# Performance work log

Hardware: AMD Instinct MI355X
Metric: run time of the kernel (lower is better)

Reference implementation:

```python
import jax, jax.numpy as jnp
import numpy as np

B, D, K = 8192, 2048, 2048  # batch, input dim, output_dim (must be equal: k==d required by call())


def setup_inputs() -> dict:
    key = jax.random.key(0)
    k1, k2, k3, k4 = jax.random.split(key, 4)
    lim_w = float(np.sqrt(6.0 / (K + D)))        # glorot_uniform for W (k,d)
    lim_v = float(np.sqrt(6.0 / (2 * D + K)))    # glorot_uniform for V (2d,k)
    return {
        "e1": jax.random.normal(k1, (B, D), jnp.float32),
        "e2": jax.random.normal(k2, (B, D), jnp.float32),
        "W": jax.random.uniform(k3, (K, D), jnp.float32, -lim_w, lim_w),
        "V": jax.random.uniform(k4, (2 * D, K), jnp.float32, -lim_v, lim_v),
        "b": jnp.zeros((K,), jnp.float32),
    }


def reference(e1, e2, W, V, b):
    # Faithful translation of the active call() of NeuralTensorDiagLayer.
    # call() tiles flatten(e1) k times and reshapes to (B, d, k); index algebra
    # shows x[p, q, r] = e1[(p*d+q)%B, r] * e2[(p*d+q)%B, r] * W[q, r]
    # (requires k == d for the W broadcast), then mean over the last axis (size k).
    # Equivalent efficient form: u = ((e1*e2) @ W.T)/k, then gather rows (p*d+q)%B.
    bsz, d = e1.shape
    k = W.shape[0]
    ff = jnp.concatenate([e1, e2], axis=-1) @ V              # (B, k) feedforward GEMM
    u = ((e1 * e2) @ W.T) / k                                # (B, k) diag bilinear, mean over k
    cols = jnp.arange(k)[None, :]                            # (1, k)
    rows = (jnp.arange(bsz)[:, None] * d + cols) % bsz       # (B, k) batch-mixing index from tile/reshape
    z = u[rows, cols]                                        # (B, k)
    return jnp.tanh(z + ff + b)
```

## Files before the change

kernel.cpp:

```cpp
#include <hip/hip_runtime.h>
#include <hip/hip_bf16.h>

typedef __bf16 bf16;
typedef bf16 bf16x8 __attribute__((ext_vector_type(8)));
typedef bf16 bf16x4 __attribute__((ext_vector_type(4)));
typedef float f32x4 __attribute__((ext_vector_type(4)));

#define AS1 __attribute__((address_space(1)))
#define AS3 __attribute__((address_space(3)))

__device__ __forceinline__ void gload_lds16(const void* g, void* l) {
    __builtin_amdgcn_global_load_lds((const AS1 void*)g, (AS3 void*)l, 16, 0, 0);
}

__device__ __forceinline__ float tanh_fast(float x) {
    float xx = fminf(fmaxf(x, -15.0f), 15.0f);
    float e = __expf(2.0f * xx);
    return (e - 1.0f) / (e + 1.0f);
}

__global__ __launch_bounds__(256) void conv_x_zs(
    const float* __restrict__ e1, const float* __restrict__ e2,
    const float* __restrict__ W, bf16* __restrict__ Xb, float* __restrict__ zs)
{
    const int r = blockIdx.x;
    const int t = threadIdx.x;
    const int c = r & 2047, m = r >> 11;
    const size_t rb = (size_t)r * 2048;

    const float4* p1 = (const float4*)(e1 + rb) + t * 2;
    const float4* p2 = (const float4*)(e2 + rb) + t * 2;
    const float4* pw = (const float4*)(W + (size_t)c * 2048) + t * 2;
    float4 a0 = p1[0], a1 = p1[1];
    float4 b0 = p2[0], b1 = p2[1];
    float4 w0 = pw[0], w1 = pw[1];

    float dot = a0.x*b0.x*w0.x + a0.y*b0.y*w0.y + a0.z*b0.z*w0.z + a0.w*b0.w*w0.w
              + a1.x*b1.x*w1.x + a1.y*b1.y*w1.y + a1.z*b1.z*w1.z + a1.w*b1.w*w1.w;

    bf16x8 xa, xb;
    xa[0]=(bf16)a0.x; xa[1]=(bf16)a0.y; xa[2]=(bf16)a0.z; xa[3]=(bf16)a0.w;
    xa[4]=(bf16)a1.x; xa[5]=(bf16)a1.y; xa[6]=(bf16)a1.z; xa[7]=(bf16)a1.w;
    xb[0]=(bf16)b0.x; xb[1]=(bf16)b0.y; xb[2]=(bf16)b0.z; xb[3]=(bf16)b0.w;
    xb[4]=(bf16)b1.x; xb[5]=(bf16)b1.y; xb[6]=(bf16)b1.z; xb[7]=(bf16)b1.w;

    *(bf16x8*)(Xb + (size_t)r * 4096 + t * 8)        = xa;
    *(bf16x8*)(Xb + (size_t)r * 4096 + 2048 + t * 8) = xb;

    #pragma unroll
    for (int off = 32; off; off >>= 1) dot += __shfl_xor(dot, off);
    __shared__ float red[4];
    if ((t & 63) == 0) red[t >> 6] = dot;
    __syncthreads();
    if (t == 0) zs[m * 2048 + c] = (red[0] + red[1] + red[2] + red[3]) * (1.0f / 2048.0f);
}

__global__ __launch_bounds__(256) void conv_vt(const float* __restrict__ V,
                                               bf16* __restrict__ Vt)
{
    __shared__ float tile[64][65];
    const int k0 = (blockIdx.x >> 5) * 64;
    const int c0 = (blockIdx.x & 31) * 64;
    const int t = threadIdx.x;
    const int rr = t >> 4;
    const int cc = (t & 15) * 4;

    #pragma unroll
    for (int r4 = 0; r4 < 4; ++r4) {
        int row = r4 * 16 + rr;
        float4 v = *(const float4*)(V + (size_t)(k0 + row) * 2048 + c0 + cc);
        tile[row][cc + 0] = v.x; tile[row][cc + 1] = v.y;
        tile[row][cc + 2] = v.z; tile[row][cc + 3] = v.w;
    }
    __syncthreads();
    #pragma unroll
    for (int r4 = 0; r4 < 4; ++r4) {
        int crow = r4 * 16 + rr;
        bf16x4 o;
        o[0] = (bf16)tile[cc + 0][crow];
        o[1] = (bf16)tile[cc + 1][crow];
        o[2] = (bf16)tile[cc + 2][crow];
        o[3] = (bf16)tile[cc + 3][crow];
        *(bf16x4*)(Vt + (size_t)(c0 + crow) * 4096 + k0 + cc) = o;
    }
}

__global__ __launch_bounds__(512, 2) void gemm_ep(
    const bf16* __restrict__ Xb, const bf16* __restrict__ Vt,
    const float* __restrict__ zs, const float* __restrict__ bias,
    float* __restrict__ out)
{
    extern __shared__ char smem[];
    const int tid  = threadIdx.x;
    const int lane = tid & 63;
    const int wid  = tid >> 6;
    const int wr = wid >> 2, wc = wid & 3;
    const int mtile = blockIdx.x >> 3;
    const int ntile = blockIdx.x & 7;
    const int row0 = mtile * 256, col0 = ntile * 256;

    const int srow = tid >> 3;
    const int scb  = ((tid & 7) * 16) ^ ((srow & 7) << 4);
    const bf16* Abase = Xb + (size_t)(row0 + srow) * 4096 + (scb >> 1);
    const bf16* Bbase = Vt + (size_t)(col0 + srow) * 4096 + (scb >> 1);

    const int lr  = lane & 15;
    const int lkb = (lane >> 4) * 16;

    f32x4 acc[2][2][4][2] = {};
    bf16x8 aA[4][2];
    bf16x8 bB[2][2][2];

    auto stage = [&](int c, int kt) {
        char* Al = smem + c * 65536 + tid * 16;
        char* Bl = smem + c * 65536 + 32768 + tid * 16;
        const bf16* Ag = Abase + (size_t)kt * 64;
        const bf16* Bg = Bbase + (size_t)kt * 64;
        #pragma unroll
        for (int r = 0; r < 4; ++r) gload_lds16(Ag + (size_t)r * 262144, Al + r * 8192);
        #pragma unroll
        for (int r = 0; r < 4; ++r) gload_lds16(Bg + (size_t)r * 262144, Bl + r * 8192);
    };

    auto ldsA = [&](const char* Ab, int qm, int i, int ks) -> bf16x8 {
        const int R = wr * 128 + qm * 64 + i * 16 + lr;
        const int cb = ks * 64 + lkb;
        return *(const bf16x8*)(Ab + R * 128 + (cb ^ ((R & 7) << 4)));
    };
    auto ldsB = [&](const char* Bb, int qn, int j, int ks) -> bf16x8 {
        const int R = wc * 64 + qn * 32 + j * 16 + lr;
        const int cb = ks * 64 + lkb;
        return *(const bf16x8*)(Bb + R * 128 + (cb ^ ((R & 7) << 4)));
    };

    auto window1 = [&](int c) {
        const char* Ab = smem + c * 65536;
        const char* Bb = smem + c * 65536 + 32768;
        #pragma unroll
        for (int i = 0; i < 4; ++i) { aA[i][0] = ldsA(Ab, 0, i, 0); aA[i][1] = ldsA(Ab, 0, i, 1); }
        #pragma unroll
        for (int j = 0; j < 2; ++j) { bB[0][j][0] = ldsB(Bb, 0, j, 0); bB[0][j][1] = ldsB(Bb, 0, j, 1); }
        __builtin_amdgcn_s_setprio(1);
        #pragma unroll
        for (int ks = 0; ks < 2; ++ks)
            #pragma unroll
            for (int i = 0; i < 4; ++i)
                #pragma unroll
                for (int j = 0; j < 2; ++j)
                    acc[0][0][i][j] = __builtin_amdgcn_mfma_f32_16x16x32_bf16(
                        aA[i][ks], bB[0][j][ks], acc[0][0][i][j], 0, 0, 0);
        __builtin_amdgcn_s_setprio(0);
        #pragma unroll
        for (int j = 0; j < 2; ++j) { bB[1][j][0] = ldsB(Bb, 1, j, 0); bB[1][j][1] = ldsB(Bb, 1, j, 1); }
        __builtin_amdgcn_s_setprio(1);
        #pragma unroll
        for (int ks = 0; ks < 2; ++ks)
            #pragma unroll
            for (int i = 0; i < 4; ++i)
                #pragma unroll
                for (int j = 0; j < 2; ++j)
                    acc[0][1][i][j] = __builtin_amdgcn_mfma_f32_16x16x32_bf16(
                        aA[i][ks], bB[1][j][ks], acc[0][1][i][j], 0, 0, 0);
        __builtin_amdgcn_s_setprio(0);
        #pragma unroll
        for (int i = 0; i < 4; ++i) { aA[i][0] = ldsA(Ab, 1, i, 0); aA[i][1] = ldsA(Ab, 1, i, 1); }
        __builtin_amdgcn_s_setprio(1);
        #pragma unroll
        for (int ks = 0; ks < 2; ++ks)
            #pragma unroll
            for (int i = 0; i < 4; ++i)
                #pragma unroll
                for (int j = 0; j < 2; ++j)
                    acc[1][1][i][j] = __builtin_amdgcn_mfma_f32_16x16x32_bf16(
                        aA[i][ks], bB[1][j][ks], acc[1][1][i][j], 0, 0, 0);
        __builtin_amdgcn_s_setprio(0);
    };

    auto mfma_q10 = [&]() {
        __builtin_amdgcn_s_setprio(1);
        #pragma unroll
        for (int ks = 0; ks < 2; ++ks)
            #pragma unroll
            for (int i = 0; i < 4; ++i)
                #pragma unroll
                for (int j = 0; j < 2; ++j)
                    acc[1][0][i][j] = __builtin_amdgcn_mfma_f32_16x16x32_bf16(
                        aA[i][ks], bB[0][j][ks], acc[1][0][i][j], 0, 0, 0);
        __builtin_amdgcn_s_setprio(0);
    };

    stage(0, 0);
    stage(1, 1);
    asm volatile("s_waitcnt vmcnt(8)" ::: "memory");
    __builtin_amdgcn_s_barrier();

    #pragma unroll 2
    for (int t = 0; t < 62; ++t) {
        const int c = t & 1;
        window1(c);
        __builtin_amdgcn_s_barrier();
        stage(c, t + 2);
        mfma_q10();
        asm volatile("s_waitcnt vmcnt(8)" ::: "memory");
        __builtin_amdgcn_s_barrier();
    }
    window1(0);
    __builtin_amdgcn_s_barrier();
    mfma_q10();
    asm volatile("s_waitcnt vmcnt(0)" ::: "memory");
    __builtin_amdgcn_s_barrier();
    window1(1);
    mfma_q10();

    const int lq = lane >> 4;
    #pragma unroll
    for (int qn = 0; qn < 2; ++qn)
        #pragma unroll
        for (int j = 0; j < 2; ++j) {
            const int ccol = col0 + wc * 64 + qn * 32 + j * 16 + lr;
            const float bb = bias[ccol];
            float zrow[4];
            #pragma unroll
            for (int q = 0; q < 4; ++q) zrow[q] = zs[q * 2048 + ccol] + bb;
            #pragma unroll
            for (int qm = 0; qm < 2; ++qm)
                #pragma unroll
                for (int i = 0; i < 4; ++i) {
                    const int prow = row0 + wr * 128 + qm * 64 + i * 16 + lq * 4;
                    #pragma unroll
                    for (int q = 0; q < 4; ++q)
                        out[(size_t)(prow + q) * 2048 + ccol] =
                            tanh_fast(acc[qm][qn][i][j][q] + zrow[q]);
                }
        }
}

extern "C" void kernel_launch(void* const* d_in, const int* in_sizes, int n_in,
                              void* d_out, int out_size, void* d_ws, size_t ws_size,
                              hipStream_t stream) {
    const float* e1 = (const float*)d_in[0];
    const float* e2 = (const float*)d_in[1];
    const float* W  = (const float*)d_in[2];
    const float* V  = (const float*)d_in[3];
    const float* b  = (const float*)d_in[4];
    float* out = (float*)d_out;

    char* ws = (char*)d_ws;
    bf16*  Xb = (bf16*)ws;
    bf16*  Vt = (bf16*)(ws + (size_t)64 * 1024 * 1024);
    float* zs = (float*)(ws + (size_t)80 * 1024 * 1024);

    conv_x_zs<<<8192, 256, 0, stream>>>(e1, e2, W, Xb, zs);
    conv_vt<<<2048, 256, 0, stream>>>(V, Vt);

    hipFuncSetAttribute((const void*)gemm_ep,
                        hipFuncAttributeMaxDynamicSharedMemorySize, 131072);
    gemm_ep<<<256, 512, 131072, stream>>>(Xb, Vt, zs, b, out);
}
```

Baseline: 169.7 us.

## Software-pipeline LDS fragment reads across K-tiles with double register buffers

Restructures the GEMM main loop so the A and B fragment reads for the next K-tile's LDS buffer are issued right after its stage becomes visible and interleaved with the current MFMA quadrants. It adds a second A register set and separate B register sets so those loads overlap compute, meant to hide LDS read latency that previously stalled before each window. The cost is more VGPR pressure from the extra fragment registers, which could reduce occupancy or cause spills. Load-address arithmetic moves to incremented pointers.

New measurement: 339.7 us. 2x slower.

```diff
diff --git a/kernel.cpp b/kernel.cpp
--- a/kernel.cpp
+++ b/kernel.cpp
@@ -108,38 +108,38 @@
     const int lkb = (lane >> 4) * 16;
 
     f32x4 acc[2][2][4][2] = {};
-    bf16x8 aA[4][2];
-    bf16x8 bB[2][2][2];
-
-    auto stage = [&](int c, int kt) {
+    bf16x8 aA[4][2], aN[4][2];
+    bf16x8 bB0[2][2], bB1[2][2];
+
+    auto stage = [&](int c, const bf16* Ag, const bf16* Bg) {
         char* Al = smem + c * 65536 + tid * 16;
         char* Bl = smem + c * 65536 + 32768 + tid * 16;
-        const bf16* Ag = Abase + (size_t)kt * 64;
-        const bf16* Bg = Bbase + (size_t)kt * 64;
         #pragma unroll
         for (int r = 0; r < 4; ++r) gload_lds16(Ag + (size_t)r * 262144, Al + r * 8192);
         #pragma unroll
         for (int r = 0; r < 4; ++r) gload_lds16(Bg + (size_t)r * 262144, Bl + r * 8192);
     };
-
-    auto ldsA = [&](const char* Ab, int qm, int i, int ks) -> bf16x8 {
-        const int R = wr * 128 + qm * 64 + i * 16 + lr;
-        const int cb = ks * 64 + lkb;
-        return *(const bf16x8*)(Ab + R * 128 + (cb ^ ((R & 7) << 4)));
-    };
-    auto ldsB = [&](const char* Bb, int qn, int j, int ks) -> bf16x8 {
-        const int R = wc * 64 + qn * 32 + j * 16 + lr;
-        const int cb = ks * 64 + lkb;
-        return *(const bf16x8*)(Bb + R * 128 + (cb ^ ((R & 7) << 4)));
-    };
-
-    auto window1 = [&](int c) {
-        const char* Ab = smem + c * 65536;
-        const char* Bb = smem + c * 65536 + 32768;
-        #pragma unroll
-        for (int i = 0; i < 4; ++i) { aA[i][0] = ldsA(Ab, 0, i, 0); aA[i][1] = ldsA(Ab, 0, i, 1); }
-        #pragma unroll
-        for (int j = 0; j < 2; ++j) { bB[0][j][0] = ldsB(Bb, 0, j, 0); bB[0][j][1] = ldsB(Bb, 0, j, 1); }
+    auto rdA = [&](bf16x8 (&dst)[4][2], const char* Ab, int half) {
+        #pragma unroll
+        for (int i = 0; i < 4; ++i)
+            #pragma unroll
+            for (int ks = 0; ks < 2; ++ks) {
+                const int R = wr * 128 + half * 64 + i * 16 + lr;
+                const int cb = ks * 64 + lkb;
+                dst[i][ks] = *(const bf16x8*)(Ab + R * 128 + (cb ^ ((R & 7) << 4)));
+            }
+    };
+    auto rdB = [&](bf16x8 (&dst)[2][2], const char* Bb, int half) {
+        #pragma unroll
+        for (int j = 0; j < 2; ++j)
+            #pragma unroll
+            for (int ks = 0; ks < 2; ++ks) {
+                const int R = wc * 64 + half * 32 + j * 16 + lr;
+                const int cb = ks * 64 + lkb;
+                dst[j][ks] = *(const bf16x8*)(Bb + R * 128 + (cb ^ ((R & 7) << 4)));
+            }
+    };
+    auto quad = [&](f32x4 (&a)[4][2], bf16x8 (&av)[4][2], bf16x8 (&bv)[2][2]) {
         __builtin_amdgcn_s_setprio(1);
         #pragma unroll
         for (int ks = 0; ks < 2; ++ks)
@@ -147,70 +147,68 @@
             for (int i = 0; i < 4; ++i)
                 #pragma unroll
                 for (int j = 0; j < 2; ++j)
-                    acc[0][0][i][j] = __builtin_amdgcn_mfma_f32_16x16x32_bf16(
-                        aA[i][ks], bB[0][j][ks], acc[0][0][i][j], 0, 0, 0);
+                    a[i][j] = __builtin_amdgcn_mfma_f32_16x16x32_bf16(
+                        av[i][ks], bv[j][ks], a[i][j], 0, 0, 0);
         __builtin_amdgcn_s_setprio(0);
-        #pragma unroll
-        for (int j = 0; j < 2; ++j) { bB[1][j][0] = ldsB(Bb, 1, j, 0); bB[1][j][1] = ldsB(Bb, 1, j, 1); }
-        __builtin_amdgcn_s_setprio(1);
-        #pragma unroll
-        for (int ks = 0; ks < 2; ++ks)
-            #pragma unroll
-            for (int i = 0; i < 4; ++i)
-                #pragma unroll
-                for (int j = 0; j < 2; ++j)
-                    acc[0][1][i][j] = __builtin_amdgcn_mfma_f32_16x16x32_bf16(
-                        aA[i][ks], bB[1][j][ks], acc[0][1][i][j], 0, 0, 0);
-        __builtin_amdgcn_s_setprio(0);
-        #pragma unroll
-        for (int i = 0; i < 4; ++i) { aA[i][0] = ldsA(Ab, 1, i, 0); aA[i][1] = ldsA(Ab, 1, i, 1); }
-        __builtin_amdgcn_s_setprio(1);
-        #pragma unroll
-        for (int ks = 0; ks < 2; ++ks)
-            #pragma unroll
-            for (int i = 0; i < 4; ++i)
-                #pragma unroll
-                for (int j = 0; j < 2; ++j)
-                    acc[1][1][i][j] = __builtin_amdgcn_mfma_f32_16x16x32_bf16(
-                        aA[i][ks], bB[1][j][ks], acc[1][1][i][j], 0, 0, 0);
-        __builtin_amdgcn_s_setprio(0);
-    };
-
-    auto mfma_q10 = [&]() {
-        __builtin_amdgcn_s_setprio(1);
-        #pragma unroll
-        for (int ks = 0; ks < 2; ++ks)
-            #pragma unroll
-            for (int i = 0; i < 4; ++i)
-                #pragma unroll
-                for (int j = 0; j < 2; ++j)
-                    acc[1][0][i][j] = __builtin_amdgcn_mfma_f32_16x16x32_bf16(
-                        aA[i][ks], bB[0][j][ks], acc[1][0][i][j], 0, 0, 0);
-        __builtin_amdgcn_s_setprio(0);
-    };
-
-    stage(0, 0);
-    stage(1, 1);
-    asm volatile("s_waitcnt vmcnt(8)" ::: "memory");
+    };
+
+    stage(0, Abase, Bbase);
+    stage(1, Abase + 64, Bbase + 64);
+    asm volatile("s_waitcnt vmcnt(0)" ::: "memory");
     __builtin_amdgcn_s_barrier();
+    rdA(aA,  smem,         0);
+    rdB(bB0, smem + 32768, 0);
+    rdB(bB1, smem + 32768, 1);
+
+    const bf16* AgS = Abase + 128;
+    const bf16* BgS = Bbase + 128;
 
     #pragma unroll 2
     for (int t = 0; t < 62; ++t) {
-        const int c = t & 1;
-        window1(c);
-        __builtin_amdgcn_s_barrier();
-        stage(c, t + 2);
-        mfma_q10();
+        const int c = t & 1, o = c ^ 1;
+        const char* Ac = smem + c * 65536;
+        const char* Ao = smem + o * 65536;
+
+        rdA(aN, Ac, 1);
+        quad(acc[0][0], aA, bB0);
+        quad(acc[0][1], aA, bB1);
+        asm volatile("s_waitcnt lgkmcnt(0)" ::: "memory");
+        __builtin_amdgcn_s_barrier();
+        stage(c, AgS, BgS);
+        AgS += 64; BgS += 64;
         asm volatile("s_waitcnt vmcnt(8)" ::: "memory");
         __builtin_amdgcn_s_barrier();
-    }
-    window1(0);
-    __builtin_amdgcn_s_barrier();
-    mfma_q10();
-    asm volatile("s_waitcnt vmcnt(0)" ::: "memory");
-    __builtin_amdgcn_s_barrier();
-    window1(1);
-    mfma_q10();
+        rdA(aA, Ao, 0);
+        quad(acc[1][1], aN, bB1);
+        rdB(bB1, Ao + 32768, 1);
+        quad(acc[1][0], aN, bB0);
+        rdB(bB0, Ao + 32768, 0);
+    }
+
+    {
+        const char* Ac = smem;
+        const char* Ao = smem + 65536;
+        rdA(aN, Ac, 1);
+        quad(acc[0][0], aA, bB0);
+        quad(acc[0][1], aA, bB1);
+        asm volatile("s_waitcnt lgkmcnt(0)" ::: "memory");
+        __builtin_amdgcn_s_barrier();
+        asm volatile("s_waitcnt vmcnt(0)" ::: "memory");
+        __builtin_amdgcn_s_barrier();
+        rdA(aA, Ao, 0);
+        quad(acc[1][1], aN, bB1);
+        rdB(bB1, Ao + 32768, 1);
+        quad(acc[1][0], aN, bB0);
+        rdB(bB0, Ao + 32768, 0);
+    }
+    {
+        const char* Ac = smem + 65536;
+        rdA(aN, Ac, 1);
+        quad(acc[0][0], aA, bB0);
+        quad(acc[0][1], aA, bB1);
+        quad(acc[1][1], aN, bB1);
+        quad(acc[1][0], aN, bB0);
+    }
 
     const int lq = lane >> 4;
     #pragma unroll
```
